# Kernel optimization log

Hardware: AMD Instinct MI355X
Metric: run time of the kernel (lower is better)

## Reference

```python
import jax, jax.numpy as jnp
import numpy as np

BIT_SHIFT = 4
PROJECT = True
DIMS = [4096, 4096, 4096, 4096]
BATCH = 8192


def ternarize(w):
    # Ternary weight quantization {-1,0,+1} with straight-through estimator.
    q = jnp.clip(jnp.round(w), -1.0, 1.0)
    return w + jax.lax.stop_gradient(q - w)


def binarize(x):
    # Binary projection sign(x) with hardtanh straight-through estimator.
    c = jnp.clip(x, -1.0, 1.0)
    return c + jax.lax.stop_gradient(jnp.sign(x) - c)


def tern_bin_layer(x, w):
    # Ternary-weight matmul followed by bit-shift scaling (divide by 2**BIT_SHIFT),
    # then optional binary projection of the activation.
    scale = 1.0 / (1 << BIT_SHIFT)
    y = jnp.matmul(x, ternarize(w)) * scale
    if PROJECT:
        y = binarize(y)
    return y


def setup_inputs() -> dict:
    key = jax.random.key(0)
    ks = jax.random.split(key, 4)
    x = jax.random.normal(ks[0], (BATCH, DIMS[0]), dtype=jnp.float32)
    # Latent float weights; ternarized inside the layer.
    W0 = jax.random.normal(ks[1], (DIMS[0], DIMS[1]), dtype=jnp.float32) * 0.7
    W1 = jax.random.normal(ks[2], (DIMS[1], DIMS[2]), dtype=jnp.float32) * 0.7
    W2 = jax.random.normal(ks[3], (DIMS[2], DIMS[3]), dtype=jnp.float32) * 0.7
    return {"x": x, "W0": W0, "W1": W1, "W2": W2}


def reference(x, W0, W1, W2):
    h = tern_bin_layer(x, W0)
    h = tern_bin_layer(h, W1)
    h = tern_bin_layer(h, W2)
    return h
```

## Files before the change

### kernel.cpp

```cpp
#include <hip/hip_runtime.h>
#include <stdint.h>

#define MDIM 8192
#define KDIM 4096
#define NDIM 4096
#define MAXFLAGS (2 * 1024 * 1024)

typedef int i32x4 __attribute__((ext_vector_type(4)));

#define VMCNT(n) asm volatile("s_waitcnt vmcnt(" #n ")" ::: "memory")
#define LGKMCNT0 asm volatile("s_waitcnt lgkmcnt(0)" ::: "memory")
#define SB0 __builtin_amdgcn_sched_barrier(0)

__device__ __forceinline__ void gl2lds16(const void* g, void* l) {
  __builtin_amdgcn_global_load_lds(
      (const __attribute__((address_space(1))) void*)(uintptr_t)(g),
      (__attribute__((address_space(3))) void*)(uintptr_t)(l), 16, 0, 0);
}

__global__ __launch_bounds__(256) void k_prep(const float* __restrict__ x,
                                              const float* __restrict__ W0,
                                              const float* __restrict__ W1,
                                              const float* __restrict__ W2,
                                              int8_t* __restrict__ Qt0,
                                              int8_t* __restrict__ Qt1,
                                              int8_t* __restrict__ Qt2,
                                              int8_t* __restrict__ dig,
                                              int* __restrict__ cnt) {
  const int bid = blockIdx.x;
  const int tid = threadIdx.x;
  if (bid == 0 && tid == 0) *cnt = 0;
  if (bid < 12288) {
    __shared__ int8_t t[64][68];
    const int wsel = bid >> 12;
    const int r = bid & 4095;
    const int n0 = (r & 63) * 64, k0 = (r >> 6) * 64;
    const float* W = (wsel == 0) ? W0 : (wsel == 1) ? W1 : W2;
    int8_t* Qt = (wsel == 0) ? Qt0 : (wsel == 1) ? Qt1 : Qt2;
    const int c4 = tid & 15, rq = tid >> 4;
#pragma unroll
    for (int i = 0; i < 4; ++i) {
      int row = i * 16 + rq;
      float4 v = *(const float4*)&W[(size_t)(k0 + row) * NDIM + n0 + c4 * 4];
      float f[4] = {v.x, v.y, v.z, v.w};
#pragma unroll
      for (int j = 0; j < 4; ++j) {
        float q = fminf(1.f, fmaxf(-1.f, rintf(f[j])));
        t[row][c4 * 4 + j] = (int8_t)(int)q;
      }
    }
    __syncthreads();
#pragma unroll
    for (int i = 0; i < 4; ++i) {
      int n = i * 16 + rq;
      char4 o;
      o.x = t[c4 * 4 + 0][n];
      o.y = t[c4 * 4 + 1][n];
      o.z = t[c4 * 4 + 2][n];
      o.w = t[c4 * 4 + 3][n];
      *(char4*)&Qt[(size_t)(n0 + n) * KDIM + k0 + c4 * 4] = o;
    }
  } else {
    const size_t P = (size_t)MDIM * KDIM;
    size_t i = ((size_t)(bid - 12288) * 256 + tid) * 4;
    float4 v = *(const float4*)(x + i);
    float f[4] = {v.x, v.y, v.z, v.w};
    int8_t dd[3][4];
#pragma unroll
    for (int j = 0; j < 4; ++j) {
      long long s = __double2ll_rn((double)f[j] * 524288.0);
      int8_t d0 = (int8_t)s; s = (s - d0) >> 8;
      int8_t d1 = (int8_t)s; s = (s - d1) >> 8;
      int8_t d2 = (int8_t)s;
      dd[0][j] = d0; dd[1][j] = d1; dd[2][j] = d2;
    }
#pragma unroll
    for (int p = 0; p < 3; ++p) {
      char4 c4v; c4v.x = dd[p][0]; c4v.y = dd[p][1]; c4v.z = dd[p][2]; c4v.w = dd[p][3];
      *(char4*)(dig + p * P + i) = c4v;
    }
  }
}

__global__ __launch_bounds__(512) void k_gemm_l1(const int8_t* __restrict__ dig,
                                                 const int8_t* __restrict__ Qt,
                                                 int8_t* __restrict__ h,
                                                 int* __restrict__ cnt,
                                                 int2* __restrict__ flags) {
  __shared__ __align__(16) int8_t As[2][3][64][128];
  __shared__ __align__(16) int8_t Bs[2][128][128];
  const int tid = threadIdx.x;
  const int w = tid >> 6, l = tid & 63;
  const size_t P = (size_t)MDIM * KDIM;

  const int nwg = gridDim.x;
  const int wg = (blockIdx.x & 7) * (nwg >> 3) + (blockIdx.x >> 3);
  const int NB = NDIM / 128;
  const int mb = wg / NB, nb = wg % NB;

  const int srow = tid >> 3;
  const int sswz = (tid & 7) ^ (srow & 7);
  const int8_t* a_src = dig + (size_t)(mb * 64 + srow) * KDIM + sswz * 16;
  const int8_t* b_src0 = Qt + (size_t)(nb * 128 + srow) * KDIM + sswz * 16;
  const int8_t* b_src1 = b_src0 + (size_t)64 * KDIM;

  i32x4 acc[3][2][2];
#pragma unroll
  for (int p = 0; p < 3; ++p)
#pragma unroll
    for (int mi = 0; mi < 2; ++mi)
#pragma unroll
      for (int ni = 0; ni < 2; ++ni) acc[p][mi][ni] = (i32x4){0, 0, 0, 0};

  const int wr = (w >> 2) * 32;
  const int wc = (w & 3) * 32;

  auto stage = [&](int buf, int kk) {
    int8_t* ad = &As[buf][0][0][0] + w * 1024;
    int8_t* bd = &Bs[buf][0][0] + w * 1024;
#pragma unroll
    for (int p = 0; p < 3; ++p) gl2lds16(a_src + p * P + kk, ad + p * 8192);
    gl2lds16(b_src0 + kk, bd);
    gl2lds16(b_src1 + kk, bd + 8192);
  };

  auto compute = [&](int buf) {
#pragma unroll
    for (int ki = 0; ki < 2; ++ki) {
      const int kg = ki * 4 + (l >> 4);
      i32x4 b[2];
#pragma unroll
      for (int ni = 0; ni < 2; ++ni) {
        int nr = wc + ni * 16 + (l & 15);
        b[ni] = *(const i32x4*)&Bs[buf][nr][(kg ^ (nr & 7)) * 16];
      }
      __builtin_amdgcn_s_setprio(1);
#pragma unroll
      for (int p = 0; p < 3; ++p)
#pragma unroll
        for (int mi = 0; mi < 2; ++mi) {
          int ar = wr + mi * 16 + (l & 15);
          i32x4 a = *(const i32x4*)&As[buf][p][ar][(kg ^ (ar & 7)) * 16];
#pragma unroll
          for (int ni = 0; ni < 2; ++ni)
            acc[p][mi][ni] =
                __builtin_amdgcn_mfma_i32_16x16x64_i8(a, b[ni], acc[p][mi][ni], 0, 0, 0);
        }
      __builtin_amdgcn_s_setprio(0);
    }
  };

  stage(0, 0);
  stage(1, 128);
  VMCNT(5);
  SB0;
  __builtin_amdgcn_s_barrier();

  const int NT = KDIM / 128;
  for (int t = 0; t < NT; ++t) {
    compute(t & 1);
    if (t == NT - 1) break;
    LGKMCNT0; SB0;
    __builtin_amdgcn_s_barrier();
    if (t + 2 < NT) {
      stage(t & 1, (t + 2) * 128);
      VMCNT(5);
    } else {
      VMCNT(0);
    }
    SB0;
    __builtin_amdgcn_s_barrier();
  }

  const int mbase = mb * 64 + wr + ((l >> 4) << 2);
  const int nbase = nb * 128 + wc + (l & 15);
#pragma unroll
  for (int mi = 0; mi < 2; ++mi)
#pragma unroll
    for (int ni = 0; ni < 2; ++ni)
#pragma unroll
      for (int j = 0; j < 4; ++j) {
        int s0 = acc[0][mi][ni][j], s1 = acc[1][mi][ni][j];
        int s2 = acc[2][mi][ni][j];
        double d = ((double)s2 * 256.0 + (double)s1) * 256.0 + (double)s0;
        int sg = (d > 0.0) - (d < 0.0);
        int row = mbase + mi * 16 + j;
        int col = nbase + ni * 16;
        h[(size_t)row * NDIM + col] = (int8_t)sg;
        if (fabs(d) <= 2048.0) {
          int idx = atomicAdd(cnt, 1);
          if (idx < MAXFLAGS) flags[idx] = make_int2(row, col);
        }
      }
}

__global__ __launch_bounds__(256) void k_fixup(const float* __restrict__ x,
                                               const int8_t* __restrict__ Qt,
                                               const int* __restrict__ cnt,
                                               const int2* __restrict__ flags,
                                               int8_t* __restrict__ h) {
  __shared__ double red[256];
  int n = *cnt;
  if (n > MAXFLAGS) n = MAXFLAGS;
  for (int i = blockIdx.x; i < n; i += gridDim.x) {
    int2 rc = flags[i];
    const float* xr = x + (size_t)rc.x * KDIM;
    const int8_t* qr = Qt + (size_t)rc.y * KDIM;
    double s = 0.0;
    for (int k = threadIdx.x; k < KDIM; k += 256)
      s += (double)xr[k] * (double)qr[k];
    red[threadIdx.x] = s;
    __syncthreads();
#pragma unroll
    for (int st = 128; st > 0; st >>= 1) {
      if (threadIdx.x < st) red[threadIdx.x] += red[threadIdx.x + st];
      __syncthreads();
    }
    if (threadIdx.x == 0) {
      double d = red[0];
      h[(size_t)rc.x * NDIM + rc.y] = (int8_t)((d > 0.0) - (d < 0.0));
    }
    __syncthreads();
  }
}

template <int F32OUT>
__global__ __launch_bounds__(512, 2) void k_gemm_bin(const int8_t* __restrict__ A,
                                                     const int8_t* __restrict__ Qt,
                                                     void* __restrict__ outp) {
  __shared__ __align__(16) int8_t smem[131072];
  const int tid = threadIdx.x;
  const int w = tid >> 6, l = tid & 63;

  const int nwg = gridDim.x;
  const int wg = (blockIdx.x & 7) * (nwg >> 3) + (blockIdx.x >> 3);
  const int NB = NDIM / 256;
  const int mb = wg / NB, nb = wg % NB;

  const int cs = ((l & 7) ^ ((l >> 3) & 7)) << 4;
  const int r0 = w * 32 + (l >> 3);
  const int8_t* gA[4];
  const int8_t* gB[4];
#pragma unroll
  for (int s = 0; s < 4; ++s) {
    gA[s] = A + (size_t)(mb * 256 + r0 + s * 8) * KDIM + cs;
    gB[s] = Qt + (size_t)(nb * 256 + r0 + s * 8) * KDIM + cs;
  }
  const int dA = w * 4096 + l * 16;

  i32x4 acc[8][4];
#pragma unroll
  for (int mi = 0; mi < 8; ++mi)
#pragma unroll
    for (int ni = 0; ni < 4; ++ni) acc[mi][ni] = (i32x4){0, 0, 0, 0};

  const int wr = (w >> 2) * 128, wc = (w & 3) * 64;

  auto stage = [&](int buf, int kk) {
    int8_t* sb = smem + buf * 65536;
#pragma unroll
    for (int s = 0; s < 4; ++s) gl2lds16(gA[s] + kk, sb + dA + s * 1024);
#pragma unroll
    for (int s = 0; s < 4; ++s) gl2lds16(gB[s] + kk, sb + 32768 + dA + s * 1024);
  };

  auto compute = [&](int buf) {
    const int8_t* sb = smem + buf * 65536;
#pragma unroll
    for (int ki = 0; ki < 2; ++ki) {
      const int kg = ki * 4 + (l >> 4);
      i32x4 b[4], a[8];
#pragma unroll
      for (int ni = 0; ni < 4; ++ni) {
        int nr = wc + ni * 16 + (l & 15);
        b[ni] = *(const i32x4*)(sb + 32768 + nr * 128 + ((kg ^ (nr & 7)) << 4));
      }
#pragma unroll
      for (int mi = 0; mi < 8; ++mi) {
        int ar = wr + mi * 16 + (l & 15);
        a[mi] = *(const i32x4*)(sb + ar * 128 + ((kg ^ (ar & 7)) << 4));
      }
      __builtin_amdgcn_s_setprio(1);
#pragma unroll
      for (int mi = 0; mi < 8; ++mi)
#pragma unroll
        for (int ni = 0; ni < 4; ++ni)
          acc[mi][ni] =
              __builtin_amdgcn_mfma_i32_16x16x64_i8(a[mi], b[ni], acc[mi][ni], 0, 0, 0);
      __builtin_amdgcn_s_setprio(0);
    }
  };

  const int NT = KDIM / 128;
  stage(0, 0); stage(1, 128);
  VMCNT(8);
  SB0;
  __builtin_amdgcn_s_barrier();

  for (int t = 0; t < NT; ++t) {
    compute(t & 1);
    if (t == NT - 1) break;
    LGKMCNT0; SB0;
    __builtin_amdgcn_s_barrier();
    if (t + 2 < NT) {
      stage(t & 1, (t + 2) * 128);
      VMCNT(8);
    } else {
      VMCNT(0);
    }
    SB0;
    __builtin_amdgcn_s_barrier();
  }

  const int mbase = mb * 256 + wr + ((l >> 4) << 2);
  const int nbase = nb * 256 + wc + (l & 15);
#pragma unroll
  for (int mi = 0; mi < 8; ++mi)
#pragma unroll
    for (int ni = 0; ni < 4; ++ni)
#pragma unroll
      for (int j = 0; j < 4; ++j) {
        int s = acc[mi][ni][j];
        int sg = (s > 0) - (s < 0);
        size_t off = (size_t)(mbase + mi * 16 + j) * NDIM + (nbase + ni * 16);
        if (F32OUT)
          ((float*)outp)[off] = (float)sg;
        else
          ((int8_t*)outp)[off] = (int8_t)sg;
      }
}

extern "C" void kernel_launch(void* const* d_in, const int* in_sizes, int n_in,
                              void* d_out, int out_size, void* d_ws, size_t ws_size,
                              hipStream_t stream) {
  (void)in_sizes; (void)n_in; (void)out_size; (void)ws_size;
  const float* x  = (const float*)d_in[0];
  const float* W0 = (const float*)d_in[1];
  const float* W1 = (const float*)d_in[2];
  const float* W2 = (const float*)d_in[3];
  float* out = (float*)d_out;

  const size_t QB = (size_t)KDIM * NDIM;
  const size_t HB = (size_t)MDIM * NDIM;
  int8_t* Qt0 = (int8_t*)d_ws;
  int8_t* Qt1 = Qt0 + QB;
  int8_t* Qt2 = Qt1 + QB;
  int8_t* h0  = Qt2 + QB;
  int8_t* h1  = h0 + HB;

  int8_t* dig = (int8_t*)d_out;
  int2* flags = (int2*)((char*)d_out + 3 * HB);
  int* cnt = (int*)((char*)d_out + 3 * HB + (size_t)MAXFLAGS * 8);

  k_prep<<<45056, 256, 0, stream>>>(x, W0, W1, W2, Qt0, Qt1, Qt2, dig, cnt);
  k_gemm_l1<<<(MDIM / 64) * (NDIM / 128), 512, 0, stream>>>(dig, Qt0, h0, cnt, flags);
  k_fixup<<<512, 256, 0, stream>>>(x, Qt0, cnt, flags, h0);
  k_gemm_bin<0><<<(MDIM / 256) * (NDIM / 256), 512, 0, stream>>>(h0, Qt1, h1);
  k_gemm_bin<1><<<(MDIM / 256) * (NDIM / 256), 512, 0, stream>>>(h1, Qt2, out);
}
```

Measured before the change: 741.3 us.

## Deepen GEMM pipelines to four 64-wide K stages with one barrier per step

Both int8 MFMA GEMM kernels switch from double-buffered 128-wide K tiles to a four-buffer ring of 64-wide K tiles, prefetching three stages ahead and issuing the next stage before computing the current one. The two barriers per iteration become a single one, and the LDS layout and swizzle are rebuilt for 64-byte rows. The layer-1 kernel also specializes its waves: six waves load the digit-plane A tiles and two waves load the B tiles. The aim is better hiding of global latency and less synchronisation, at the cost of more iterations with less MFMA work per barrier and a smaller LDS footprint for the bin kernel.

```diff
diff --git a/kernel.cpp b/kernel.cpp
--- a/kernel.cpp
+++ b/kernel.cpp
@@ -87,8 +87,7 @@
                                                  int8_t* __restrict__ h,
                                                  int* __restrict__ cnt,
                                                  int2* __restrict__ flags) {
-  __shared__ __align__(16) int8_t As[2][3][64][128];
-  __shared__ __align__(16) int8_t Bs[2][128][128];
+  __shared__ __align__(16) int8_t smem[81920];
   const int tid = threadIdx.x;
   const int w = tid >> 6, l = tid & 63;
   const size_t P = (size_t)MDIM * KDIM;
@@ -98,11 +97,22 @@
   const int NB = NDIM / 128;
   const int mb = wg / NB, nb = wg % NB;
 
-  const int srow = tid >> 3;
-  const int sswz = (tid & 7) ^ (srow & 7);
-  const int8_t* a_src = dig + (size_t)(mb * 64 + srow) * KDIM + sswz * 16;
-  const int8_t* b_src0 = Qt + (size_t)(nb * 128 + srow) * KDIM + sswz * 16;
-  const int8_t* b_src1 = b_src0 + (size_t)64 * KDIM;
+  const int srow_in = l >> 2;
+  const int scol = (((l & 3) ^ ((l >> 3) & 3)) << 4);
+  const bool wA = (w < 6);
+  const int8_t *ga0 = nullptr, *ga1 = nullptr;
+  const int8_t *gb0 = nullptr, *gb1 = nullptr, *gb2 = nullptr, *gb3 = nullptr;
+  if (wA) {
+    int i0 = 2 * w, i1 = 2 * w + 1;
+    ga0 = dig + (size_t)(i0 >> 2) * P + (size_t)(mb * 64 + (i0 & 3) * 16 + srow_in) * KDIM + scol;
+    ga1 = dig + (size_t)(i1 >> 2) * P + (size_t)(mb * 64 + (i1 & 3) * 16 + srow_in) * KDIM + scol;
+  } else {
+    int j = (w - 6) * 4;
+    gb0 = Qt + (size_t)(nb * 128 + (j + 0) * 16 + srow_in) * KDIM + scol;
+    gb1 = Qt + (size_t)(nb * 128 + (j + 1) * 16 + srow_in) * KDIM + scol;
+    gb2 = Qt + (size_t)(nb * 128 + (j + 2) * 16 + srow_in) * KDIM + scol;
+    gb3 = Qt + (size_t)(nb * 128 + (j + 3) * 16 + srow_in) * KDIM + scol;
+  }
 
   i32x4 acc[3][2][2];
 #pragma unroll
@@ -114,57 +124,62 @@
 
   const int wr = (w >> 2) * 32;
   const int wc = (w & 3) * 32;
+  const int kg = l >> 4;
 
   auto stage = [&](int buf, int kk) {
-    int8_t* ad = &As[buf][0][0][0] + w * 1024;
-    int8_t* bd = &Bs[buf][0][0] + w * 1024;
-#pragma unroll
-    for (int p = 0; p < 3; ++p) gl2lds16(a_src + p * P + kk, ad + p * 8192);
-    gl2lds16(b_src0 + kk, bd);
-    gl2lds16(b_src1 + kk, bd + 8192);
+    int8_t* sb = smem + buf * 20480;
+    if (wA) {
+      int8_t* d0 = sb + (2 * w) * 1024;
+      gl2lds16(ga0 + kk, d0);
+      gl2lds16(ga1 + kk, d0 + 1024);
+    } else {
+      int8_t* d0 = sb + 12288 + ((w - 6) * 4) * 1024;
+      gl2lds16(gb0 + kk, d0);
+      gl2lds16(gb1 + kk, d0 + 1024);
+      gl2lds16(gb2 + kk, d0 + 2048);
+      gl2lds16(gb3 + kk, d0 + 3072);
+    }
   };
 
   auto compute = [&](int buf) {
-#pragma unroll
-    for (int ki = 0; ki < 2; ++ki) {
-      const int kg = ki * 4 + (l >> 4);
-      i32x4 b[2];
-#pragma unroll
-      for (int ni = 0; ni < 2; ++ni) {
-        int nr = wc + ni * 16 + (l & 15);
-        b[ni] = *(const i32x4*)&Bs[buf][nr][(kg ^ (nr & 7)) * 16];
+    const int8_t* sb = smem + buf * 20480;
+    i32x4 b[2];
+#pragma unroll
+    for (int ni = 0; ni < 2; ++ni) {
+      int nr = wc + ni * 16 + (l & 15);
+      b[ni] = *(const i32x4*)(sb + 12288 + nr * 64 + ((kg ^ ((nr >> 1) & 3)) << 4));
+    }
+    __builtin_amdgcn_s_setprio(1);
+#pragma unroll
+    for (int p = 0; p < 3; ++p)
+#pragma unroll
+      for (int mi = 0; mi < 2; ++mi) {
+        int ar = wr + mi * 16 + (l & 15);
+        i32x4 a = *(const i32x4*)(sb + p * 4096 + ar * 64 + ((kg ^ ((ar >> 1) & 3)) << 4));
+#pragma unroll
+        for (int ni = 0; ni < 2; ++ni)
+          acc[p][mi][ni] =
+              __builtin_amdgcn_mfma_i32_16x16x64_i8(a, b[ni], acc[p][mi][ni], 0, 0, 0);
       }
-      __builtin_amdgcn_s_setprio(1);
-#pragma unroll
-      for (int p = 0; p < 3; ++p)
-#pragma unroll
-        for (int mi = 0; mi < 2; ++mi) {
-          int ar = wr + mi * 16 + (l & 15);
-          i32x4 a = *(const i32x4*)&As[buf][p][ar][(kg ^ (ar & 7)) * 16];
-#pragma unroll
-          for (int ni = 0; ni < 2; ++ni)
-            acc[p][mi][ni] =
-                __builtin_amdgcn_mfma_i32_16x16x64_i8(a, b[ni], acc[p][mi][ni], 0, 0, 0);
-        }
-      __builtin_amdgcn_s_setprio(0);
-    }
+    __builtin_amdgcn_s_setprio(0);
   };
 
-  stage(0, 0);
-  stage(1, 128);
-  VMCNT(5);
+  const int NT = KDIM / 64;
+  stage(0, 0); stage(1, 64); stage(2, 128);
+  if (wA) VMCNT(4); else VMCNT(8);
   SB0;
   __builtin_amdgcn_s_barrier();
 
-  const int NT = KDIM / 128;
   for (int t = 0; t < NT; ++t) {
-    compute(t & 1);
+    if (t + 3 < NT) stage((t + 3) & 3, (t + 3) * 64);
+    SB0;
+    compute(t & 3);
     if (t == NT - 1) break;
-    LGKMCNT0; SB0;
-    __builtin_amdgcn_s_barrier();
-    if (t + 2 < NT) {
-      stage(t & 1, (t + 2) * 128);
-      VMCNT(5);
+    LGKMCNT0;
+    if (t + 3 < NT) {
+      if (wA) VMCNT(4); else VMCNT(8);
+    } else if (t + 2 < NT) {
+      if (wA) VMCNT(2); else VMCNT(4);
     } else {
       VMCNT(0);
     }
@@ -237,16 +252,15 @@
   const int NB = NDIM / 256;
   const int mb = wg / NB, nb = wg % NB;
 
-  const int cs = ((l & 7) ^ ((l >> 3) & 7)) << 4;
-  const int r0 = w * 32 + (l >> 3);
-  const int8_t* gA[4];
-  const int8_t* gB[4];
-#pragma unroll
-  for (int s = 0; s < 4; ++s) {
-    gA[s] = A + (size_t)(mb * 256 + r0 + s * 8) * KDIM + cs;
-    gB[s] = Qt + (size_t)(nb * 256 + r0 + s * 8) * KDIM + cs;
-  }
-  const int dA = w * 4096 + l * 16;
+  const int srow_in = l >> 2;
+  const int scol = (((l & 3) ^ ((l >> 3) & 3)) << 4);
+  const int8_t* gA[2];
+  const int8_t* gB[2];
+#pragma unroll
+  for (int s = 0; s < 2; ++s) {
+    gA[s] = A + (size_t)(mb * 256 + (2 * w + s) * 16 + srow_in) * KDIM + scol;
+    gB[s] = Qt + (size_t)(nb * 256 + (2 * w + s) * 16 + srow_in) * KDIM + scol;
+  }
 
   i32x4 acc[8][4];
 #pragma unroll
@@ -255,56 +269,56 @@
     for (int ni = 0; ni < 4; ++ni) acc[mi][ni] = (i32x4){0, 0, 0, 0};
 
   const int wr = (w >> 2) * 128, wc = (w & 3) * 64;
+  const int kg = l >> 4;
 
   auto stage = [&](int buf, int kk) {
-    int8_t* sb = smem + buf * 65536;
-#pragma unroll
-    for (int s = 0; s < 4; ++s) gl2lds16(gA[s] + kk, sb + dA + s * 1024);
-#pragma unroll
-    for (int s = 0; s < 4; ++s) gl2lds16(gB[s] + kk, sb + 32768 + dA + s * 1024);
+    int8_t* sb = smem + buf * 32768;
+#pragma unroll
+    for (int s = 0; s < 2; ++s) {
+      gl2lds16(gA[s] + kk, sb + (2 * w + s) * 1024);
+      gl2lds16(gB[s] + kk, sb + 16384 + (2 * w + s) * 1024);
+    }
   };
 
   auto compute = [&](int buf) {
-    const int8_t* sb = smem + buf * 65536;
-#pragma unroll
-    for (int ki = 0; ki < 2; ++ki) {
-      const int kg = ki * 4 + (l >> 4);
-      i32x4 b[4], a[8];
-#pragma unroll
-      for (int ni = 0; ni < 4; ++ni) {
-        int nr = wc + ni * 16 + (l & 15);
-        b[ni] = *(const i32x4*)(sb + 32768 + nr * 128 + ((kg ^ (nr & 7)) << 4));
-      }
-#pragma unroll
-      for (int mi = 0; mi < 8; ++mi) {
-        int ar = wr + mi * 16 + (l & 15);
-        a[mi] = *(const i32x4*)(sb + ar * 128 + ((kg ^ (ar & 7)) << 4));
-      }
-      __builtin_amdgcn_s_setprio(1);
-#pragma unroll
-      for (int mi = 0; mi < 8; ++mi)
-#pragma unroll
-        for (int ni = 0; ni < 4; ++ni)
-          acc[mi][ni] =
-              __builtin_amdgcn_mfma_i32_16x16x64_i8(a[mi], b[ni], acc[mi][ni], 0, 0, 0);
-      __builtin_amdgcn_s_setprio(0);
-    }
+    const int8_t* sb = smem + buf * 32768;
+    i32x4 b[4], a[8];
+#pragma unroll
+    for (int ni = 0; ni < 4; ++ni) {
+      int nr = wc + ni * 16 + (l & 15);
+      b[ni] = *(const i32x4*)(sb + 16384 + nr * 64 + ((kg ^ ((nr >> 1) & 3)) << 4));
+    }
+#pragma unroll
+    for (int mi = 0; mi < 8; ++mi) {
+      int ar = wr + mi * 16 + (l & 15);
+      a[mi] = *(const i32x4*)(sb + ar * 64 + ((kg ^ ((ar >> 1) & 3)) << 4));
+    }
+    __builtin_amdgcn_s_setprio(1);
+#pragma unroll
+    for (int mi = 0; mi < 8; ++mi)
+#pragma unroll
+      for (int ni = 0; ni < 4; ++ni)
+        acc[mi][ni] =
+            __builtin_amdgcn_mfma_i32_16x16x64_i8(a[mi], b[ni], acc[mi][ni], 0, 0, 0);
+    __builtin_amdgcn_s_setprio(0);
   };
 
-  const int NT = KDIM / 128;
-  stage(0, 0); stage(1, 128);
+  const int NT = KDIM / 64;
+  stage(0, 0); stage(1, 64); stage(2, 128);
   VMCNT(8);
   SB0;
   __builtin_amdgcn_s_barrier();
 
   for (int t = 0; t < NT; ++t) {
-    compute(t & 1);
+    if (t + 3 < NT) stage((t + 3) & 3, (t + 3) * 64);
+    SB0;
+    compute(t & 3);
     if (t == NT - 1) break;
-    LGKMCNT0; SB0;
-    __builtin_amdgcn_s_barrier();
-    if (t + 2 < NT) {
-      stage(t & 1, (t + 2) * 128);
+    LGKMCNT0;
+    if (t + 3 < NT) {
       VMCNT(8);
+    } else if (t + 2 < NT) {
+      VMCNT(4);
     } else {
       VMCNT(0);
     }
```

After: 816.3 us. +10.1%, slower.

## Switch int8 GEMM to 64-wide K tiles with four-stage LDS pipeline

Applied to the files above, without the earlier changes.

Changes the main loop from two 128-deep K stages to a four-buffer ring of 64-deep stages, issuing the next stage's global-to-LDS loads before computing the current one. The LDS swizzle is redone for 64-byte rows and staging now uses 4 loads per thread per stage. The goal is deeper prefetch and less exposed load latency. The cost is more loop iterations, more barriers per unit of work, and fewer MFMAs between synchronisations.

```diff
diff --git a/kernel.cpp b/kernel.cpp
--- a/kernel.cpp
+++ b/kernel.cpp
@@ -237,16 +237,15 @@
   const int NB = NDIM / 256;
   const int mb = wg / NB, nb = wg % NB;
 
-  const int cs = ((l & 7) ^ ((l >> 3) & 7)) << 4;
-  const int r0 = w * 32 + (l >> 3);
-  const int8_t* gA[4];
-  const int8_t* gB[4];
-#pragma unroll
-  for (int s = 0; s < 4; ++s) {
-    gA[s] = A + (size_t)(mb * 256 + r0 + s * 8) * KDIM + cs;
-    gB[s] = Qt + (size_t)(nb * 256 + r0 + s * 8) * KDIM + cs;
-  }
-  const int dA = w * 4096 + l * 16;
+  const int srow_in = l >> 2;
+  const int scol = (((l & 3) ^ ((l >> 3) & 3)) << 4);
+  const int8_t* gA[2];
+  const int8_t* gB[2];
+#pragma unroll
+  for (int s = 0; s < 2; ++s) {
+    gA[s] = A + (size_t)(mb * 256 + (2 * w + s) * 16 + srow_in) * KDIM + scol;
+    gB[s] = Qt + (size_t)(nb * 256 + (2 * w + s) * 16 + srow_in) * KDIM + scol;
+  }
 
   i32x4 acc[8][4];
 #pragma unroll
@@ -255,56 +254,56 @@
     for (int ni = 0; ni < 4; ++ni) acc[mi][ni] = (i32x4){0, 0, 0, 0};
 
   const int wr = (w >> 2) * 128, wc = (w & 3) * 64;
+  const int kg = l >> 4;
 
   auto stage = [&](int buf, int kk) {
-    int8_t* sb = smem + buf * 65536;
-#pragma unroll
-    for (int s = 0; s < 4; ++s) gl2lds16(gA[s] + kk, sb + dA + s * 1024);
-#pragma unroll
-    for (int s = 0; s < 4; ++s) gl2lds16(gB[s] + kk, sb + 32768 + dA + s * 1024);
+    int8_t* sb = smem + buf * 32768;
+#pragma unroll
+    for (int s = 0; s < 2; ++s) {
+      gl2lds16(gA[s] + kk, sb + (2 * w + s) * 1024);
+      gl2lds16(gB[s] + kk, sb + 16384 + (2 * w + s) * 1024);
+    }
   };
 
   auto compute = [&](int buf) {
-    const int8_t* sb = smem + buf * 65536;
-#pragma unroll
-    for (int ki = 0; ki < 2; ++ki) {
-      const int kg = ki * 4 + (l >> 4);
-      i32x4 b[4], a[8];
-#pragma unroll
-      for (int ni = 0; ni < 4; ++ni) {
-        int nr = wc + ni * 16 + (l & 15);
-        b[ni] = *(const i32x4*)(sb + 32768 + nr * 128 + ((kg ^ (nr & 7)) << 4));
-      }
-#pragma unroll
-      for (int mi = 0; mi < 8; ++mi) {
-        int ar = wr + mi * 16 + (l & 15);
-        a[mi] = *(const i32x4*)(sb + ar * 128 + ((kg ^ (ar & 7)) << 4));
-      }
-      __builtin_amdgcn_s_setprio(1);
-#pragma unroll
-      for (int mi = 0; mi < 8; ++mi)
-#pragma unroll
-        for (int ni = 0; ni < 4; ++ni)
-          acc[mi][ni] =
-              __builtin_amdgcn_mfma_i32_16x16x64_i8(a[mi], b[ni], acc[mi][ni], 0, 0, 0);
-      __builtin_amdgcn_s_setprio(0);
-    }
+    const int8_t* sb = smem + buf * 32768;
+    i32x4 b[4], a[8];
+#pragma unroll
+    for (int ni = 0; ni < 4; ++ni) {
+      int nr = wc + ni * 16 + (l & 15);
+      b[ni] = *(const i32x4*)(sb + 16384 + nr * 64 + ((kg ^ ((nr >> 1) & 3)) << 4));
+    }
+#pragma unroll
+    for (int mi = 0; mi < 8; ++mi) {
+      int ar = wr + mi * 16 + (l & 15);
+      a[mi] = *(const i32x4*)(sb + ar * 64 + ((kg ^ ((ar >> 1) & 3)) << 4));
+    }
+    __builtin_amdgcn_s_setprio(1);
+#pragma unroll
+    for (int mi = 0; mi < 8; ++mi)
+#pragma unroll
+      for (int ni = 0; ni < 4; ++ni)
+        acc[mi][ni] =
+            __builtin_amdgcn_mfma_i32_16x16x64_i8(a[mi], b[ni], acc[mi][ni], 0, 0, 0);
+    __builtin_amdgcn_s_setprio(0);
   };
 
-  const int NT = KDIM / 128;
-  stage(0, 0); stage(1, 128);
+  const int NT = KDIM / 64;
+  stage(0, 0); stage(1, 64); stage(2, 128);
   VMCNT(8);
   SB0;
   __builtin_amdgcn_s_barrier();
 
   for (int t = 0; t < NT; ++t) {
-    compute(t & 1);
+    if (t + 3 < NT) stage((t + 3) & 3, (t + 3) * 64);
+    SB0;
+    compute(t & 3);
     if (t == NT - 1) break;
-    LGKMCNT0; SB0;
-    __builtin_amdgcn_s_barrier();
-    if (t + 2 < NT) {
-      stage(t & 1, (t + 2) * 128);
+    LGKMCNT0;
+    if (t + 3 < NT) {
       VMCNT(8);
+    } else if (t + 2 < NT) {
+      VMCNT(4);
     } else {
       VMCNT(0);
     }
```

Result: no change. 735.6 us (-0.8%).
